# Performance work log

Hardware: AMD Instinct MI355X
Metric: run time of the kernel (lower is better)

The kernel has to match this reference:

```python
import jax, jax.numpy as jnp
import numpy as np

RRELU_SLOPE = (1.0 / 8.0 + 1.0 / 3.0) / 2.0  # F.rrelu eval mode
N_ENT, N_REL2, H, E, B, T = 20000, 460, 128, 400000, 1024, 8


def _lin(x, W, b):
    return x @ W.T + b  # torch nn.Linear convention


def _gru_cell(x, h, w_ih, w_hh, b_ih, b_hh):
    gi = x @ w_ih.T + b_ih
    gh = h @ w_hh.T + b_hh
    i_r, i_z, i_n = jnp.split(gi, 3, axis=1)
    h_r, h_z, h_n = jnp.split(gh, 3, axis=1)
    r = jax.nn.sigmoid(i_r + h_r)
    z = jax.nn.sigmoid(i_z + h_z)
    n = jnp.tanh(i_n + r * h_n)
    return (1.0 - z) * n + z * h


def setup_inputs() -> dict:
    key = jax.random.key(0)
    ks = jax.random.split(key, 24)
    s = 0.02
    inp = {
        'ent_emb': jax.random.normal(ks[0], (N_ENT, H), jnp.float32),
        'rel_emb': jax.random.normal(ks[1], (N_REL2, H), jnp.float32),
        'weight_neighbor': jax.random.normal(ks[2], (H, H), jnp.float32) * s,
        'loop_weight': jax.random.normal(ks[3], (H, H), jnp.float32) * s,
        'evolve_loop_weight': jax.random.normal(ks[4], (H, H), jnp.float32) * s,
        'w_ih': jax.random.normal(ks[5], (3 * H, H), jnp.float32) * s,
        'w_hh': jax.random.normal(ks[6], (3 * H, H), jnp.float32) * s,
        'b_ih': jnp.zeros((3 * H,), jnp.float32),
        'b_hh': jnp.zeros((3 * H,), jnp.float32),
        'W_map1': jax.random.normal(ks[7], (2 * H, H), jnp.float32) * s,
        'b_map1': jnp.zeros((2 * H,), jnp.float32),
        'W_map2': jax.random.normal(ks[8], (H, 2 * H), jnp.float32) * s,
        'b_map2': jnp.zeros((H,), jnp.float32),
        'W_h1': jax.random.normal(ks[9], (H, H), jnp.float32) * s,
        'b_h1': jnp.zeros((H,), jnp.float32),
        'W_h2': jax.random.normal(ks[10], (H, H), jnp.float32) * s,
        'b_h2': jnp.zeros((H,), jnp.float32),
        'W_align': jax.random.normal(ks[11], (H, H), jnp.float32) * s,
        'b_align': jnp.zeros((H,), jnp.float32),
        'W_attn': jax.random.normal(ks[12], (H, H), jnp.float32) * s,
        'b_attn': jnp.zeros((H,), jnp.float32),
    }
    u = jax.random.uniform(ks[13], (B, T * N_REL2), jnp.float32)
    mask = jax.random.uniform(ks[14], (B, T * N_REL2)) > 0.7  # sparse history
    inp['partial_embeding'] = u * mask
    inp['edge_src'] = jax.random.randint(ks[15], (E,), 0, N_ENT, jnp.int32)
    inp['edge_dst'] = jax.random.randint(ks[16], (E,), 0, N_ENT, jnp.int32)
    inp['edge_type'] = jax.random.randint(ks[17], (E,), 0, N_REL2, jnp.int32)
    sub = jax.random.randint(ks[18], (B,), 0, N_ENT, jnp.int32)
    rel = jax.random.randint(ks[19], (B,), 0, N_REL2, jnp.int32)
    obj = jax.random.randint(ks[20], (B,), 0, N_ENT, jnp.int32)
    inp['triples'] = jnp.stack([sub, rel, obj], axis=1)
    return inp


def reference(ent_emb, rel_emb, weight_neighbor, loop_weight, evolve_loop_weight,
              w_ih, w_hh, b_ih, b_hh, W_map1, b_map1, W_map2, b_map2,
              W_h1, b_h1, W_h2, b_h2, W_align, b_align, W_attn, b_attn,
              partial_embeding, edge_src, edge_dst, edge_type, triples):
    # ---- UnionRGCNLayer: gather-transform-scatter ----
    h = ent_emb
    msg = (h[edge_src] + rel_emb[edge_type]) @ weight_neighbor          # [E, H]
    agg = jax.ops.segment_sum(msg, edge_dst, num_segments=N_ENT)        # [N, H]
    deg = jax.ops.segment_sum(jnp.ones((edge_dst.shape[0],), h.dtype), edge_dst,
                              num_segments=N_ENT)
    norm = jnp.where(deg > 0, 1.0 / jnp.where(deg > 0, deg, 1.0), 0.0)[:, None]
    loop = jnp.where((deg > 0)[:, None], h @ loop_weight, h @ evolve_loop_weight)
    x = agg * norm + loop
    pre_emb = jnp.where(x >= 0, x, x * RRELU_SLOPE)                     # rrelu (eval)

    # ---- PathPredictor.forward_back ----
    mapped_rel = _lin(_lin(rel_emb, W_map1, b_map1), W_map2, b_map2)    # [2R, H]
    q_rel = mapped_rel[triples[:, 1]]                                   # [B, H]
    A = _lin(q_rel, W_attn, b_attn) @ mapped_rel.T                      # [B, 2R]
    hist = partial_embeding.reshape(B, T, N_REL2).transpose(1, 0, 2)    # [T, B, 2R]

    def step(gh, cur):
        attn = cur * A
        attn = jax.nn.softmax(jnp.where(attn == 0, -1e9, attn), axis=1)
        rel_path = attn @ mapped_rel                                    # [B, H]
        return _gru_cell(rel_path, gh, w_ih, w_hh, b_ih, b_hh), None

    gru_hidden, _ = jax.lax.scan(step, jnp.zeros((B, H), pre_emb.dtype), hist)
    predicted_hist = 0.1 * _lin(_lin(q_rel, W_h1, b_h1), W_h2, b_h2) + q_rel
    match_loss = jnp.mean((predicted_hist - gru_hidden) ** 2)

    # ---- forward_forth, distmult scoring ----
    gh2 = _gru_cell(q_rel, predicted_hist, w_ih, w_hh, b_ih, b_hh)      # [B, H]
    sub_emb = pre_emb[triples[:, 0]]
    aligned_all = _lin(pre_emb, W_align, b_align)                       # [N, H]
    score_ = (_lin(sub_emb, W_align, b_align) * gh2) @ aligned_all.T    # [B, N]
    score = jax.nn.sigmoid(score_)
    # BCE(score, one_hot(obj)) without materializing labels:
    logp = jax.nn.log_sigmoid(score_)
    log1mp = jax.nn.log_sigmoid(-score_)
    total = -jnp.sum(log1mp)
    rows = jnp.arange(B)
    total = total + jnp.sum(log1mp[rows, triples[:, 2]] - logp[rows, triples[:, 2]])
    path_loss = total / (B * N_ENT)
    return score, match_loss, path_loss
```

## Files before the change

### kernel.cpp

```cpp
#include <hip/hip_runtime.h>

typedef unsigned short u16;
typedef unsigned int u32;
typedef __attribute__((ext_vector_type(8))) short bf8v;
typedef __attribute__((ext_vector_type(4))) float f4v;

#define RRELU_SLOPE 0.22916666667f

__device__ inline float bf2f(u16 u){ unsigned int i = ((unsigned int)u) << 16; float f; __builtin_memcpy(&f, &i, 4); return f; }
__device__ inline u16 f2bf(float f){ unsigned int i; __builtin_memcpy(&i, &f, 4); unsigned int r = (i + 0x7fffu + ((i >> 16) & 1u)) >> 16; return (u16)r; }
__device__ inline float frcp(float x){ return __builtin_amdgcn_rcpf(x); }
__device__ inline float fsigm(float x){ return frcp(1.f + __expf(-x)); }
__device__ inline float ftanh(float x){ return 2.f * frcp(1.f + __expf(-2.f * x)) - 1.f; }

__global__ __launch_bounds__(256) void prep_k(
    const float* __restrict__ Wn, const float* __restrict__ Wl, const float* __restrict__ We,
    const float* __restrict__ wih, const float* __restrict__ whh,
    const float* __restrict__ m1, const float* __restrict__ m2,
    const float* __restrict__ h1, const float* __restrict__ h2,
    const float* __restrict__ attn, const float* __restrict__ alg, const float* __restrict__ rel,
    u16* __restrict__ Bcat, u16* __restrict__ wihb, u16* __restrict__ whhb,
    u16* __restrict__ m1b, u16* __restrict__ m2b, u16* __restrict__ h1b, u16* __restrict__ h2b,
    u16* __restrict__ attnb, u16* __restrict__ algb, u16* __restrict__ relb)
{
    int id = blockIdx.x * 256 + threadIdx.x;
    if (id < 49152) {
        int n = id / 384, k = id % 384;
        float v = (k < 128) ? Wn[k*128 + n] : (k < 256 ? Wl[(k-128)*128 + n] : We[(k-256)*128 + n]);
        Bcat[id] = f2bf(v); return;
    }
    id -= 49152;
    if (id < 49152) { wihb[id] = f2bf(wih[id]); return; } id -= 49152;
    if (id < 49152) { whhb[id] = f2bf(whh[id]); return; } id -= 49152;
    if (id < 32768) { m1b[id]  = f2bf(m1[id]);  return; } id -= 32768;
    if (id < 32768) { m2b[id]  = f2bf(m2[id]);  return; } id -= 32768;
    if (id < 16384) { h1b[id]  = f2bf(h1[id]);  return; } id -= 16384;
    if (id < 16384) { h2b[id]  = f2bf(h2[id]);  return; } id -= 16384;
    if (id < 16384) { attnb[id]= f2bf(attn[id]);return; } id -= 16384;
    if (id < 16384) { algb[id] = f2bf(alg[id]); return; } id -= 16384;
    if (id < 58880) { relb[id] = f2bf(rel[id]); return; }
}

__global__ __launch_bounds__(256) void entcast_k(
    const float* __restrict__ ent, u16* __restrict__ entb)
{
    int id = blockIdx.x * 256 + threadIdx.x;
    entb[id] = f2bf(ent[id]);
}

__global__ __launch_bounds__(256) void hist_k(
    const int* __restrict__ dst, int* __restrict__ hist, int E)
{
    int e = blockIdx.x * 256 + threadIdx.x;
    if (e < E) atomicAdd(&hist[dst[e]], 1);
}

__global__ __launch_bounds__(1024) void scan_k(
    const int* __restrict__ hist, int* __restrict__ starts, int* __restrict__ cursor)
{
    __shared__ int part[1024];
    int t = threadIdx.x;
    int base = t * 20;
    int s = 0;
    for (int j = 0; j < 20; ++j) { int idx = base + j; if (idx < 20000) s += hist[idx]; }
    part[t] = s;
    __syncthreads();
    for (int off = 1; off < 1024; off <<= 1) {
        int v = (t >= off) ? part[t - off] : 0;
        __syncthreads();
        part[t] += v;
        __syncthreads();
    }
    int run = (t > 0) ? part[t - 1] : 0;
    for (int j = 0; j < 20; ++j) {
        int idx = base + j;
        if (idx < 20000) { starts[idx] = run; cursor[idx] = run; run += hist[idx]; }
    }
    if (t == 1023) starts[20000] = run;
}

__global__ __launch_bounds__(256) void scatter_k(
    const int* __restrict__ src, const int* __restrict__ dst, const int* __restrict__ typ,
    int* __restrict__ cursor, int2* __restrict__ spack, int E)
{
    int e = blockIdx.x * 256 + threadIdx.x;
    if (e >= E) return;
    int d = dst[e];
    int p = atomicAdd(&cursor[d], 1);
    spack[p] = make_int2(src[e], typ[e]);
}

__global__ __launch_bounds__(64) void agg_acat_k(
    const int2* __restrict__ spack, const int* __restrict__ starts,
    const u32* __restrict__ hb, const u32* __restrict__ rb, u32* __restrict__ Acat32)
{
    int i = blockIdx.x;
    int lane = threadIdx.x;
    int s0 = starts[i], s1 = starts[i + 1];
    float sx = 0.f, sy = 0.f;
    for (int e = s0; e < s1; ++e) {
        int2 st = spack[e];
        u32 a = hb[(long)st.x * 64 + lane];
        u32 r = rb[(long)st.y * 64 + lane];
        sx += bf2f((u16)(a & 0xffff)) + bf2f((u16)(r & 0xffff));
        sy += bf2f((u16)(a >> 16))    + bf2f((u16)(r >> 16));
    }
    bool has = s1 > s0;
    float nrm = has ? frcp((float)(s1 - s0)) : 0.f;
    u32 hv = hb[(long)i * 64 + lane];
    u32 agg = (u32)f2bf(sx * nrm) | ((u32)f2bf(sy * nrm) << 16);
    long o = (long)i * 192 + lane;
    Acat32[o]       = agg;
    Acat32[o + 64]  = has ? hv : 0u;
    Acat32[o + 128] = has ? 0u : hv;
}

__global__ __launch_bounds__(256) void gemm_nt(
    const u16* __restrict__ A, const u16* __restrict__ B, const float* __restrict__ bias,
    float* __restrict__ Cf, u16* __restrict__ Cbf, u16* __restrict__ CT,
    const u16* __restrict__ residb, const int* __restrict__ arows,
    int M, int N, int K, int lda, int ldb, int ldc, int ldct, int arow_stride,
    float rscale, int epi)
{
    int tid = threadIdx.x;
    int wave = tid >> 6, lane = tid & 63;
    int ln = lane & 15, q = lane >> 4;
    int bm = blockIdx.y * 64 + wave * 16;
    int bn = blockIdx.x * 64;
    int am = bm + ln; if (am >= M) am = M - 1;
    long ar = arows ? (long)arows[(long)am * arow_stride] : (long)am;
    const u16* Ap = A + ar * lda;
    int br[4];
#pragma unroll
    for (int nt = 0; nt < 4; ++nt) { int n = bn + nt*16 + ln; br[nt] = (n < N) ? n : (N - 1); }
    f4v acc[4] = {};
    for (int kc = 0; kc < K; kc += 32) {
        bf8v af = *(const bf8v*)(Ap + kc + q*8);
#pragma unroll
        for (int nt = 0; nt < 4; ++nt) {
            bf8v bv = *(const bf8v*)(B + (long)br[nt]*ldb + kc + q*8);
            acc[nt] = __builtin_amdgcn_mfma_f32_16x16x32_bf16(af, bv, acc[nt], 0, 0, 0);
        }
    }
#pragma unroll
    for (int nt = 0; nt < 4; ++nt) {
        int n = bn + nt*16 + ln;
        if (n >= N) continue;
        float bv = bias ? bias[n] : 0.f;
#pragma unroll
        for (int r = 0; r < 4; ++r) {
            int m = bm + q*4 + r;
            if (m >= M) continue;
            float v = acc[nt][r] + bv;
            if (epi == 1) v = (v >= 0.f) ? v : v * RRELU_SLOPE;
            if (residb)  v = rscale * v + bf2f(residb[(long)m*ldc + n]);
            long ci = (long)m*ldc + n;
            if (Cf)  Cf[ci]  = v;
            if (Cbf) Cbf[ci] = f2bf(v);
            if (CT)  CT[(long)n*ldct + m] = f2bf(v);
        }
    }
}

__global__ __launch_bounds__(256) void qrel_k(
    const u16* __restrict__ mapb, const int* __restrict__ trip,
    u16* __restrict__ qrelb, u16* __restrict__ X)
{
    int id = blockIdx.x * 256 + threadIdx.x;
    int b = id >> 7, k = id & 127;
    int r = trip[b*3 + 1];
    u16 v = mapb[r*128 + k];
    qrelb[id] = v;
    X[(long)(8192 + b)*128 + k] = v;
}

__global__ __launch_bounds__(64) void softmax_k(
    const float* __restrict__ Amat, const float* __restrict__ part, u16* __restrict__ Xattn)
{
    int row = blockIdx.x;
    int t = row >> 10, b = row & 1023;
    int lane = threadIdx.x;
    const float* arow = Amat + (long)b*460;
    const float* crow = part + (long)b*3680 + t*460;
    float v[8], e[8];
    float m = -1e30f;
#pragma unroll
    for (int i = 0; i < 8; ++i) {
        int r = i*64 + lane;
        e[i] = 0.f;
        if (r < 460) {
            float x = crow[r] * arow[r];
            x = (x == 0.f) ? -1e9f : x;
            v[i] = x; m = fmaxf(m, x);
        } else v[i] = -1e30f;
    }
#pragma unroll
    for (int off = 32; off; off >>= 1) m = fmaxf(m, __shfl_xor(m, off));
    float sum = 0.f;
#pragma unroll
    for (int i = 0; i < 8; ++i) {
        int r = i*64 + lane;
        if (r < 460) { e[i] = __expf(v[i] - m); sum += e[i]; }
    }
#pragma unroll
    for (int off = 32; off; off >>= 1) sum += __shfl_xor(sum, off);
    float inv = frcp(sum);
#pragma unroll
    for (int i = 0; i < 8; ++i) {
        int r = i*64 + lane;
        if (r < 460)      Xattn[(long)row*480 + r] = f2bf(e[i] * inv);
        else if (r < 480) Xattn[(long)row*480 + r] = 0;
    }
}

__global__ __launch_bounds__(256) void gru_k(
    const float* __restrict__ gi, const u16* __restrict__ whhb, const float* __restrict__ bhh,
    const float* __restrict__ pred, float* __restrict__ gh2, float* __restrict__ match_acc)
{
    __shared__ u16  hbf[16][136];
    __shared__ float hf [4][128];
    __shared__ float ghl[4][388];
    __shared__ float red[4];
    int tid = threadIdx.x;
    int wave = tid >> 6, lane = tid & 63;
    int ln = lane & 15, q = lane >> 4;
    int bb = blockIdx.x * 4;
    for (int i = tid; i < 16*136; i += 256) hbf[i/136][i%136] = 0;
    for (int i = tid; i < 4*128; i += 256) hf[i>>7][i&127] = 0.f;
    bf8v bfrag[6][4];
#pragma unroll
    for (int nt = 0; nt < 6; ++nt)
#pragma unroll
        for (int kc = 0; kc < 4; ++kc)
            bfrag[nt][kc] = *(const bf8v*)(whhb + (long)(wave*96 + nt*16 + ln)*128 + kc*32 + q*8);
    int k = tid & 127;
    float br = bhh[k], bz = bhh[128 + k], bn_ = bhh[256 + k];
    __syncthreads();
    float msum = 0.f;
    for (int t = 0; t <= 8; ++t) {
        float gr[2], gz[2], gn[2], pv[2];
        long girow0 = (t < 8) ? ((long)t*1024 + bb) : (8192 + bb);
#pragma unroll
        for (int it = 0; it < 2; ++it) {
            int m = it*2 + (tid >> 7);
            const float* gp = gi + (girow0 + m)*384;
            gr[it] = gp[k]; gz[it] = gp[128 + k]; gn[it] = gp[256 + k];
            pv[it] = (t >= 7) ? pred[(long)(bb + m)*128 + k] : 0.f;
        }
        if (t == 8) {
#pragma unroll
            for (int it = 0; it < 2; ++it) {
                int m = it*2 + (tid >> 7);
                hf[m][k] = pv[it]; hbf[m][k] = f2bf(pv[it]);
            }
            __syncthreads();
        }
        f4v acc[6] = {};
#pragma unroll
        for (int kc = 0; kc < 4; ++kc) {
            bf8v af = *(const bf8v*)&hbf[ln][kc*32 + q*8];
#pragma unroll
            for (int nt = 0; nt < 6; ++nt)
                acc[nt] = __builtin_amdgcn_mfma_f32_16x16x32_bf16(af, bfrag[nt][kc], acc[nt], 0, 0, 0);
        }
        if (q == 0) {
#pragma unroll
            for (int nt = 0; nt < 6; ++nt)
#pragma unroll
                for (int r = 0; r < 4; ++r)
                    ghl[r][wave*96 + nt*16 + ln] = acc[nt][r];
        }
        __syncthreads();
#pragma unroll
        for (int it = 0; it < 2; ++it) {
            int m = it*2 + (tid >> 7);
            float rr = fsigm(gr[it] + ghl[m][k] + br);
            float zz = fsigm(gz[it] + ghl[m][128 + k] + bz);
            float nn = ftanh(gn[it] + rr * (ghl[m][256 + k] + bn_));
            float hn = (1.f - zz) * nn + zz * hf[m][k];
            if (t == 7) { float d = pv[it] - hn; msum += d*d; }
            if (t == 8) { gh2[(long)(bb + m)*128 + k] = hn; }
            else        { hf[m][k] = hn; hbf[m][k] = f2bf(hn); }
        }
        __syncthreads();
    }
#pragma unroll
    for (int off = 32; off; off >>= 1) msum += __shfl_down(msum, off);
    if (lane == 0) red[wave] = msum;
    __syncthreads();
    if (tid == 0) atomicAdd(match_acc, red[0] + red[1] + red[2] + red[3]);
}

__global__ __launch_bounds__(256) void vmul_k(
    const float* __restrict__ subl, const float* __restrict__ gh2, u16* __restrict__ V)
{
    int id = blockIdx.x * 256 + threadIdx.x;
    V[id] = f2bf(subl[id] * gh2[id]);
}

__global__ __launch_bounds__(512) void score_k(
    const u16* __restrict__ V, const u16* __restrict__ AL,
    float* __restrict__ out, float* __restrict__ sp_acc, int N)
{
    int tid = threadIdx.x;
    int wave = tid >> 6, lane = tid & 63;
    int ln = lane & 15, q = lane >> 4;
    int bm = blockIdx.y * 128 + (wave >> 2) * 64;
    int bn = blockIdx.x * 128 + (wave & 3) * 32;
    int br[2];
#pragma unroll
    for (int nt = 0; nt < 2; ++nt) { int n = bn + nt*16 + ln; br[nt] = (n < N) ? n : (N - 1); }
    f4v acc[4][2] = {};
    for (int kc = 0; kc < 128; kc += 32) {
        bf8v a[4], b[2];
#pragma unroll
        for (int mt = 0; mt < 4; ++mt)
            a[mt] = *(const bf8v*)(V + (long)(bm + mt*16 + ln)*128 + kc + q*8);
#pragma unroll
        for (int nt = 0; nt < 2; ++nt)
            b[nt] = *(const bf8v*)(AL + (long)br[nt]*128 + kc + q*8);
#pragma unroll
        for (int mt = 0; mt < 4; ++mt)
#pragma unroll
            for (int nt = 0; nt < 2; ++nt)
                acc[mt][nt] = __builtin_amdgcn_mfma_f32_16x16x32_bf16(a[mt], b[nt], acc[mt][nt], 0, 0, 0);
    }
    float lsum = 0.f;
#pragma unroll
    for (int mt = 0; mt < 4; ++mt)
#pragma unroll
    for (int nt = 0; nt < 2; ++nt) {
        int n = bn + nt*16 + ln;
        if (n >= N) continue;
#pragma unroll
        for (int r = 0; r < 4; ++r) {
            int m = bm + mt*16 + q*4 + r;
            float s = acc[mt][nt][r];
            float e = __expf(-fabsf(s));
            float d = 1.f + e;
            float inv = frcp(d);
            __builtin_nontemporal_store((s >= 0.f) ? inv : e * inv, &out[(long)m*N + n]);
            lsum += fmaxf(s, 0.f) + __logf(d);
        }
    }
#pragma unroll
    for (int off = 32; off; off >>= 1) lsum += __shfl_xor(lsum, off);
    __shared__ float red[8];
    if (lane == 0) red[wave] = lsum;
    __syncthreads();
    if (tid == 0) {
        float tsum = 0.f;
#pragma unroll
        for (int w = 0; w < 8; ++w) tsum += red[w];
        atomicAdd(sp_acc, tsum);
    }
}

__global__ __launch_bounds__(64) void objdot_k(
    const u16* __restrict__ V, const u16* __restrict__ AL, const int* __restrict__ trip,
    float* __restrict__ obj_acc)
{
    int b = blockIdx.x, lane = threadIdx.x;
    int obj = trip[b*3 + 2];
    const u16* v = V + (long)b*128;
    const u16* a = AL + (long)obj*128;
    float s = 0.f;
    for (int k = lane; k < 128; k += 64) s += bf2f(v[k]) * bf2f(a[k]);
    for (int off = 32; off; off >>= 1) s += __shfl_down(s, off);
    if (lane == 0) atomicAdd(obj_acc, -s);
}

__global__ void final_k(const float* __restrict__ acc, float* __restrict__ out)
{
    out[20480000] = acc[0] / (1024.f * 128.f);
    out[20480001] = (acc[1] + acc[2]) / (1024.f * 20000.f);
}

extern "C" void kernel_launch(void* const* d_in, const int* in_sizes, int n_in,
                              void* d_out, int out_size, void* d_ws, size_t ws_size,
                              hipStream_t stream)
{
    const float* ent  = (const float*)d_in[0];
    const float* rel  = (const float*)d_in[1];
    const float* Wn   = (const float*)d_in[2];
    const float* Wl   = (const float*)d_in[3];
    const float* We   = (const float*)d_in[4];
    const float* wih  = (const float*)d_in[5];
    const float* whh  = (const float*)d_in[6];
    const float* b_ih = (const float*)d_in[7];
    const float* b_hh = (const float*)d_in[8];
    const float* Wm1  = (const float*)d_in[9];
    const float* bm1  = (const float*)d_in[10];
    const float* Wm2  = (const float*)d_in[11];
    const float* bm2  = (const float*)d_in[12];
    const float* Wh1  = (const float*)d_in[13];
    const float* bh1  = (const float*)d_in[14];
    const float* Wh2  = (const float*)d_in[15];
    const float* bh2  = (const float*)d_in[16];
    const float* Wal  = (const float*)d_in[17];
    const float* bal  = (const float*)d_in[18];
    const float* Wat  = (const float*)d_in[19];
    const float* bat  = (const float*)d_in[20];
    const float* part = (const float*)d_in[21];
    const int* esrc   = (const int*)d_in[22];
    const int* edst   = (const int*)d_in[23];
    const int* etyp   = (const int*)d_in[24];
    const int* trip   = (const int*)d_in[25];
    float* out = (float*)d_out;
    const int E = in_sizes[22];

    char* ws = (char*)d_ws;
    size_t off = 0;
    auto alloc = [&](size_t bytes) { size_t o = off; off = (off + bytes + 255) & ~(size_t)255; return o; };

    size_t o_acc   = alloc(256);
    size_t o_hist  = alloc(20000 * 4);
    size_t o_mapT  = alloc(128 * 480 * 2);
    size_t zend = off;
    size_t o_starts= alloc(20004 * 4);
    size_t o_cur   = alloc(20000 * 4);
    size_t o_spack = alloc((size_t)E * 8);
    size_t o_entb  = alloc((size_t)20000 * 128 * 2);
    size_t o_acat  = alloc((size_t)20000 * 384 * 2);
    size_t o_pre   = alloc((size_t)20000 * 128 * 2);
    size_t o_aln   = alloc((size_t)20000 * 128 * 2);
    size_t o_bcat  = alloc(128 * 384 * 2);
    size_t o_wih   = alloc(384 * 128 * 2);
    size_t o_whh   = alloc(384 * 128 * 2);
    size_t o_m1    = alloc(256 * 128 * 2);
    size_t o_m2    = alloc(128 * 256 * 2);
    size_t o_h1    = alloc(128 * 128 * 2);
    size_t o_h2    = alloc(128 * 128 * 2);
    size_t o_at    = alloc(128 * 128 * 2);
    size_t o_al    = alloc(128 * 128 * 2);
    size_t o_rel   = alloc(460 * 128 * 2);
    size_t o_t1    = alloc(460 * 256 * 2);
    size_t o_map   = alloc(460 * 128 * 2);
    size_t o_qrel  = alloc(1024 * 128 * 2);
    size_t o_atq   = alloc(1024 * 128 * 2);
    size_t o_th1   = alloc(1024 * 128 * 2);
    size_t o_pred  = alloc(1024 * 128 * 4);
    size_t o_amat  = alloc((size_t)1024 * 460 * 4);
    size_t o_xat   = alloc((size_t)8192 * 480 * 2);
    size_t o_X     = alloc((size_t)9216 * 128 * 2);
    size_t o_gi    = alloc((size_t)9216 * 384 * 4);
    size_t o_subl  = alloc(1024 * 128 * 4);
    size_t o_gh2   = alloc(1024 * 128 * 4);
    size_t o_V     = alloc(1024 * 128 * 2);

    float* accp  = (float*)(ws + o_acc);
    int* histp   = (int*)(ws + o_hist);
    u16* mapT    = (u16*)(ws + o_mapT);
    int* startsp = (int*)(ws + o_starts);
    int* curp    = (int*)(ws + o_cur);
    int2* spack  = (int2*)(ws + o_spack);
    u16* entb    = (u16*)(ws + o_entb);
    u16* acat    = (u16*)(ws + o_acat);
    u16* preb    = (u16*)(ws + o_pre);
    u16* alnb    = (u16*)(ws + o_aln);
    u16* bcat    = (u16*)(ws + o_bcat);
    u16* wihb    = (u16*)(ws + o_wih);
    u16* whhb    = (u16*)(ws + o_whh);
    u16* m1b     = (u16*)(ws + o_m1);
    u16* m2b     = (u16*)(ws + o_m2);
    u16* h1b     = (u16*)(ws + o_h1);
    u16* h2b     = (u16*)(ws + o_h2);
    u16* atb     = (u16*)(ws + o_at);
    u16* alb     = (u16*)(ws + o_al);
    u16* relb    = (u16*)(ws + o_rel);
    u16* t1b     = (u16*)(ws + o_t1);
    u16* mapb    = (u16*)(ws + o_map);
    u16* qrelb   = (u16*)(ws + o_qrel);
    u16* atqb    = (u16*)(ws + o_atq);
    u16* th1b    = (u16*)(ws + o_th1);
    float* predf = (float*)(ws + o_pred);
    float* amat  = (float*)(ws + o_amat);
    u16* xat     = (u16*)(ws + o_xat);
    u16* Xb      = (u16*)(ws + o_X);
    float* gif   = (float*)(ws + o_gi);
    float* subl  = (float*)(ws + o_subl);
    float* gh2f  = (float*)(ws + o_gh2);
    u16* Vb      = (u16*)(ws + o_V);

    hipMemsetAsync(ws, 0, zend, stream);

    prep_k<<<1318, 256, 0, stream>>>(Wn, Wl, We, wih, whh, Wm1, Wm2, Wh1, Wh2, Wat, Wal, rel,
                                     bcat, wihb, whhb, m1b, m2b, h1b, h2b, atb, alb, relb);
    entcast_k<<<10000, 256, 0, stream>>>(ent, entb);

    int eb = (E + 255) / 256;
    hist_k<<<eb, 256, 0, stream>>>(edst, histp, E);
    scan_k<<<1, 1024, 0, stream>>>(histp, startsp, curp);
    scatter_k<<<eb, 256, 0, stream>>>(esrc, edst, etyp, curp, spack, E);
    agg_acat_k<<<20000, 64, 0, stream>>>(spack, startsp, (const u32*)entb, (const u32*)relb, (u32*)acat);

    gemm_nt<<<dim3(2, 313), 256, 0, stream>>>(acat, bcat, nullptr, nullptr, preb, nullptr, nullptr, nullptr,
                                              20000, 128, 384, 384, 384, 128, 0, 0, 0.f, 1);
    gemm_nt<<<dim3(2, 313), 256, 0, stream>>>(preb, alb, bal, nullptr, alnb, nullptr, nullptr, nullptr,
                                              20000, 128, 128, 128, 128, 128, 0, 0, 0.f, 0);
    gemm_nt<<<dim3(4, 8), 256, 0, stream>>>(relb, m1b, bm1, nullptr, t1b, nullptr, nullptr, nullptr,
                                            460, 256, 128, 128, 128, 256, 0, 0, 0.f, 0);
    gemm_nt<<<dim3(2, 8), 256, 0, stream>>>(t1b, m2b, bm2, nullptr, mapb, mapT, nullptr, nullptr,
                                            460, 128, 256, 256, 256, 128, 480, 0, 0.f, 0);

    qrel_k<<<512, 256, 0, stream>>>(mapb, trip, qrelb, Xb);

    gemm_nt<<<dim3(2, 16), 256, 0, stream>>>(qrelb, atb, bat, nullptr, atqb, nullptr, nullptr, nullptr,
                                             1024, 128, 128, 128, 128, 128, 0, 0, 0.f, 0);
    gemm_nt<<<dim3(2, 16), 256, 0, stream>>>(qrelb, h1b, bh1, nullptr, th1b, nullptr, nullptr, nullptr,
                                             1024, 128, 128, 128, 128, 128, 0, 0, 0.f, 0);
    gemm_nt<<<dim3(2, 16), 256, 0, stream>>>(th1b, h2b, bh2, predf, nullptr, nullptr, qrelb, nullptr,
                                             1024, 128, 128, 128, 128, 128, 0, 0, 0.1f, 0);
    gemm_nt<<<dim3(8, 16), 256, 0, stream>>>(atqb, mapb, nullptr, amat, nullptr, nullptr, nullptr, nullptr,
                                             1024, 460, 128, 128, 128, 460, 0, 0, 0.f, 0);

    softmax_k<<<8192, 64, 0, stream>>>(amat, part, xat);

    gemm_nt<<<dim3(2, 128), 256, 0, stream>>>(xat, mapT, nullptr, nullptr, Xb, nullptr, nullptr, nullptr,
                                              8192, 128, 480, 480, 480, 128, 0, 0, 0.f, 0);
    gemm_nt<<<dim3(6, 144), 256, 0, stream>>>(Xb, wihb, b_ih, gif, nullptr, nullptr, nullptr, nullptr,
                                              9216, 384, 128, 128, 128, 384, 0, 0, 0.f, 0);
    gemm_nt<<<dim3(2, 16), 256, 0, stream>>>(preb, alb, bal, subl, nullptr, nullptr, nullptr, trip,
                                             1024, 128, 128, 128, 128, 128, 0, 3, 0.f, 0);

    gru_k<<<256, 256, 0, stream>>>(gif, whhb, b_hh, predf, gh2f, accp + 0);

    vmul_k<<<512, 256, 0, stream>>>(subl, gh2f, Vb);

    score_k<<<dim3(157, 8), 512, 0, stream>>>(Vb, alnb, out, accp + 1, 20000);

    objdot_k<<<1024, 64, 0, stream>>>(Vb, alnb, trip, accp + 2);

    final_k<<<1, 1, 0, stream>>>(accp, out);

    (void)in_sizes; (void)n_in; (void)out_size; (void)ws_size;
}
```

Measured before the change: 482.0 us.

## Stage score tile in LDS for vectorized stores and fuse small kernels

The score kernel now writes sigmoid outputs into a per-wave LDS tile and then emits row-contiguous float4 nontemporal stores, replacing scattered per-element writes. The entity cast is folded into the prep kernel, the attention and h1 projections are merged into one wider GEMM with a concatenated bias, and the V product is fused with the object dot-product. This targets output-store inefficiency and launch overhead. The 64KB LDS staging buffer may limit occupancy of the score kernel.

```diff
diff --git a/kernel.cpp b/kernel.cpp
--- a/kernel.cpp
+++ b/kernel.cpp
@@ -19,9 +19,11 @@
     const float* __restrict__ m1, const float* __restrict__ m2,
     const float* __restrict__ h1, const float* __restrict__ h2,
     const float* __restrict__ attn, const float* __restrict__ alg, const float* __restrict__ rel,
+    const float* __restrict__ ent, const float* __restrict__ bat, const float* __restrict__ bh1,
     u16* __restrict__ Bcat, u16* __restrict__ wihb, u16* __restrict__ whhb,
     u16* __restrict__ m1b, u16* __restrict__ m2b, u16* __restrict__ h1b, u16* __restrict__ h2b,
-    u16* __restrict__ attnb, u16* __restrict__ algb, u16* __restrict__ relb)
+    u16* __restrict__ attnb, u16* __restrict__ algb, u16* __restrict__ relb,
+    u16* __restrict__ entb, float* __restrict__ bias2)
 {
     int id = blockIdx.x * 256 + threadIdx.x;
     if (id < 49152) {
@@ -38,14 +40,9 @@
     if (id < 16384) { h2b[id]  = f2bf(h2[id]);  return; } id -= 16384;
     if (id < 16384) { attnb[id]= f2bf(attn[id]);return; } id -= 16384;
     if (id < 16384) { algb[id] = f2bf(alg[id]); return; } id -= 16384;
-    if (id < 58880) { relb[id] = f2bf(rel[id]); return; }
-}
-
-__global__ __launch_bounds__(256) void entcast_k(
-    const float* __restrict__ ent, u16* __restrict__ entb)
-{
-    int id = blockIdx.x * 256 + threadIdx.x;
-    entb[id] = f2bf(ent[id]);
+    if (id < 58880) { relb[id] = f2bf(rel[id]); return; } id -= 58880;
+    if (id < 2560000) { entb[id] = f2bf(ent[id]); return; } id -= 2560000;
+    if (id < 256) { bias2[id] = (id < 128) ? bat[id] : bh1[id - 128]; }
 }
 
 __global__ __launch_bounds__(256) void hist_k(
@@ -291,22 +288,35 @@
     if (tid == 0) atomicAdd(match_acc, red[0] + red[1] + red[2] + red[3]);
 }
 
-__global__ __launch_bounds__(256) void vmul_k(
-    const float* __restrict__ subl, const float* __restrict__ gh2, u16* __restrict__ V)
-{
-    int id = blockIdx.x * 256 + threadIdx.x;
-    V[id] = f2bf(subl[id] * gh2[id]);
+__global__ __launch_bounds__(128) void vo_k(
+    const float* __restrict__ subl, const float* __restrict__ gh2,
+    const u16* __restrict__ AL, const int* __restrict__ trip,
+    u16* __restrict__ V, float* __restrict__ obj_acc)
+{
+    int b = blockIdx.x, k = threadIdx.x;
+    u16 vb = f2bf(subl[b*128 + k] * gh2[b*128 + k]);
+    V[b*128 + k] = vb;
+    int obj = trip[b*3 + 2];
+    float s = bf2f(vb) * bf2f(AL[(long)obj*128 + k]);
+#pragma unroll
+    for (int off = 32; off; off >>= 1) s += __shfl_down(s, off);
+    __shared__ float red2[2];
+    if ((k & 63) == 0) red2[k >> 6] = s;
+    __syncthreads();
+    if (k == 0) atomicAdd(obj_acc, -(red2[0] + red2[1]));
 }
 
 __global__ __launch_bounds__(512) void score_k(
     const u16* __restrict__ V, const u16* __restrict__ AL,
     float* __restrict__ out, float* __restrict__ sp_acc, int N)
 {
+    __shared__ float stage[8][2048];
     int tid = threadIdx.x;
     int wave = tid >> 6, lane = tid & 63;
     int ln = lane & 15, q = lane >> 4;
     int bm = blockIdx.y * 128 + (wave >> 2) * 64;
     int bn = blockIdx.x * 128 + (wave & 3) * 32;
+    bool valid = bn < N;
     int br[2];
 #pragma unroll
     for (int nt = 0; nt < 2; ++nt) { int n = bn + nt*16 + ln; br[nt] = (n < N) ? n : (N - 1); }
@@ -326,21 +336,28 @@
                 acc[mt][nt] = __builtin_amdgcn_mfma_f32_16x16x32_bf16(a[mt], b[nt], acc[mt][nt], 0, 0, 0);
     }
     float lsum = 0.f;
+    float* st = stage[wave];
 #pragma unroll
     for (int mt = 0; mt < 4; ++mt)
 #pragma unroll
-    for (int nt = 0; nt < 2; ++nt) {
-        int n = bn + nt*16 + ln;
-        if (n >= N) continue;
-#pragma unroll
-        for (int r = 0; r < 4; ++r) {
-            int m = bm + mt*16 + q*4 + r;
-            float s = acc[mt][nt][r];
-            float e = __expf(-fabsf(s));
-            float d = 1.f + e;
-            float inv = frcp(d);
-            __builtin_nontemporal_store((s >= 0.f) ? inv : e * inv, &out[(long)m*N + n]);
-            lsum += fmaxf(s, 0.f) + __logf(d);
+    for (int nt = 0; nt < 2; ++nt)
+#pragma unroll
+    for (int r = 0; r < 4; ++r) {
+        float s = acc[mt][nt][r];
+        float e = __expf(-fabsf(s));
+        float d = 1.f + e;
+        float inv = frcp(d);
+        st[(mt*16 + q*4 + r)*32 + nt*16 + ln] = (s >= 0.f) ? inv : e * inv;
+        lsum += fmaxf(s, 0.f) + __logf(d);
+    }
+    if (!valid) lsum = 0.f;
+    if (valid) {
+        int row0 = lane >> 3, c4 = (lane & 7) << 2;
+#pragma unroll
+        for (int i = 0; i < 8; ++i) {
+            int row = i*8 + row0;
+            f4v vv = *(const f4v*)&st[row*32 + c4];
+            __builtin_nontemporal_store(vv, (f4v*)&out[(long)(bm + row)*N + bn + c4]);
         }
     }
 #pragma unroll
@@ -354,20 +371,6 @@
         for (int w = 0; w < 8; ++w) tsum += red[w];
         atomicAdd(sp_acc, tsum);
     }
-}
-
-__global__ __launch_bounds__(64) void objdot_k(
-    const u16* __restrict__ V, const u16* __restrict__ AL, const int* __restrict__ trip,
-    float* __restrict__ obj_acc)
-{
-    int b = blockIdx.x, lane = threadIdx.x;
-    int obj = trip[b*3 + 2];
-    const u16* v = V + (long)b*128;
-    const u16* a = AL + (long)obj*128;
-    float s = 0.f;
-    for (int k = lane; k < 128; k += 64) s += bf2f(v[k]) * bf2f(a[k]);
-    for (int off = 32; off; off >>= 1) s += __shfl_down(s, off);
-    if (lane == 0) atomicAdd(obj_acc, -s);
 }
 
 __global__ void final_k(const float* __restrict__ acc, float* __restrict__ out)
@@ -429,16 +432,15 @@
     size_t o_whh   = alloc(384 * 128 * 2);
     size_t o_m1    = alloc(256 * 128 * 2);
     size_t o_m2    = alloc(128 * 256 * 2);
-    size_t o_h1    = alloc(128 * 128 * 2);
+    size_t o_ath   = alloc(2 * 128 * 128 * 2);
     size_t o_h2    = alloc(128 * 128 * 2);
-    size_t o_at    = alloc(128 * 128 * 2);
     size_t o_al    = alloc(128 * 128 * 2);
     size_t o_rel   = alloc(460 * 128 * 2);
     size_t o_t1    = alloc(460 * 256 * 2);
     size_t o_map   = alloc(460 * 128 * 2);
     size_t o_qrel  = alloc(1024 * 128 * 2);
-    size_t o_atq   = alloc(1024 * 128 * 2);
-    size_t o_th1   = alloc(1024 * 128 * 2);
+    size_t o_qt    = alloc((size_t)1024 * 256 * 2);
+    size_t o_b2    = alloc(256 * 4);
     size_t o_pred  = alloc(1024 * 128 * 4);
     size_t o_amat  = alloc((size_t)1024 * 460 * 4);
     size_t o_xat   = alloc((size_t)8192 * 480 * 2);
@@ -463,16 +465,16 @@
     u16* whhb    = (u16*)(ws + o_whh);
     u16* m1b     = (u16*)(ws + o_m1);
     u16* m2b     = (u16*)(ws + o_m2);
-    u16* h1b     = (u16*)(ws + o_h1);
+    u16* atb     = (u16*)(ws + o_ath);
+    u16* h1b     = atb + 128 * 128;
     u16* h2b     = (u16*)(ws + o_h2);
-    u16* atb     = (u16*)(ws + o_at);
     u16* alb     = (u16*)(ws + o_al);
     u16* relb    = (u16*)(ws + o_rel);
     u16* t1b     = (u16*)(ws + o_t1);
     u16* mapb    = (u16*)(ws + o_map);
     u16* qrelb   = (u16*)(ws + o_qrel);
-    u16* atqb    = (u16*)(ws + o_atq);
-    u16* th1b    = (u16*)(ws + o_th1);
+    u16* qtb     = (u16*)(ws + o_qt);
+    float* bias2 = (float*)(ws + o_b2);
     float* predf = (float*)(ws + o_pred);
     float* amat  = (float*)(ws + o_amat);
     u16* xat     = (u16*)(ws + o_xat);
@@ -484,9 +486,10 @@
 
     hipMemsetAsync(ws, 0, zend, stream);
 
-    prep_k<<<1318, 256, 0, stream>>>(Wn, Wl, We, wih, whh, Wm1, Wm2, Wh1, Wh2, Wat, Wal, rel,
-                                     bcat, wihb, whhb, m1b, m2b, h1b, h2b, atb, alb, relb);
-    entcast_k<<<10000, 256, 0, stream>>>(ent, entb);
+    prep_k<<<11319, 256, 0, stream>>>(Wn, Wl, We, wih, whh, Wm1, Wm2, Wh1, Wh2, Wat, Wal, rel,
+                                      ent, bat, bh1,
+                                      bcat, wihb, whhb, m1b, m2b, h1b, h2b, atb, alb, relb,
+                                      entb, bias2);
 
     int eb = (E + 255) / 256;
     hist_k<<<eb, 256, 0, stream>>>(edst, histp, E);
@@ -505,14 +508,12 @@
 
     qrel_k<<<512, 256, 0, stream>>>(mapb, trip, qrelb, Xb);
 
-    gemm_nt<<<dim3(2, 16), 256, 0, stream>>>(qrelb, atb, bat, nullptr, atqb, nullptr, nullptr, nullptr,
-                                             1024, 128, 128, 128, 128, 128, 0, 0, 0.f, 0);
-    gemm_nt<<<dim3(2, 16), 256, 0, stream>>>(qrelb, h1b, bh1, nullptr, th1b, nullptr, nullptr, nullptr,
-                                             1024, 128, 128, 128, 128, 128, 0, 0, 0.f, 0);
-    gemm_nt<<<dim3(2, 16), 256, 0, stream>>>(th1b, h2b, bh2, predf, nullptr, nullptr, qrelb, nullptr,
-                                             1024, 128, 128, 128, 128, 128, 0, 0, 0.1f, 0);
-    gemm_nt<<<dim3(8, 16), 256, 0, stream>>>(atqb, mapb, nullptr, amat, nullptr, nullptr, nullptr, nullptr,
-                                             1024, 460, 128, 128, 128, 460, 0, 0, 0.f, 0);
+    gemm_nt<<<dim3(4, 16), 256, 0, stream>>>(qrelb, atb, bias2, nullptr, qtb, nullptr, nullptr, nullptr,
+                                             1024, 256, 128, 128, 128, 256, 0, 0, 0.f, 0);
+    gemm_nt<<<dim3(2, 16), 256, 0, stream>>>(qtb + 128, h2b, bh2, predf, nullptr, nullptr, qrelb, nullptr,
+                                             1024, 128, 128, 256, 128, 128, 0, 0, 0.1f, 0);
+    gemm_nt<<<dim3(8, 16), 256, 0, stream>>>(qtb, mapb, nullptr, amat, nullptr, nullptr, nullptr, nullptr,
+                                             1024, 460, 128, 256, 128, 460, 0, 0, 0.f, 0);
 
     softmax_k<<<8192, 64, 0, stream>>>(amat, part, xat);
 
@@ -525,12 +526,10 @@
 
     gru_k<<<256, 256, 0, stream>>>(gif, whhb, b_hh, predf, gh2f, accp + 0);
 
-    vmul_k<<<512, 256, 0, stream>>>(subl, gh2f, Vb);
+    vo_k<<<1024, 128, 0, stream>>>(subl, gh2f, alnb, trip, Vb, accp + 2);
 
     score_k<<<dim3(157, 8), 512, 0, stream>>>(Vb, alnb, out, accp + 1, 20000);
 
-    objdot_k<<<1024, 64, 0, stream>>>(Vb, alnb, trip, accp + 2);
-
     final_k<<<1, 1, 0, stream>>>(accp, out);
 
     (void)in_sizes; (void)n_in; (void)out_size; (void)ws_size;
```

Result: faster. 470.4 us (-2.4%).
